# Kernel optimization log

Hardware: AMD Instinct MI355X
Metric: run time of the kernel (lower is better)

Reference implementation:

```python
import jax, jax.numpy as jnp
import numpy as np

EPSILON = 1e-6
SEARCH_RADIUS = 11 // 2  # search_window_size=11 -> 121 shifts
PATCH_RADIUS = 5 // 2    # patch_size=5 box sum


def shift_stack(t, r):
    # Matches ShiftStack: outer loop x_shift, inner loop y_shift, roll dims (H,W)=(2,3).
    # t: [B,C,H,W] -> [B,C,H,W,(2r+1)^2]
    return jnp.stack(
        [jnp.roll(t, (dy, dx), axis=(2, 3))
         for dx in range(-r, r + 1) for dy in range(-r, r + 1)],
        axis=-1,
    )


def box_sum(t, r):
    # Circular box-filter sum over a (2r+1)x(2r+1) window; separable form is
    # mathematically identical to the original 25 rolls (rolls commute/add).
    s = sum(jnp.roll(t, d, axis=2) for d in range(-r, r + 1))
    return sum(jnp.roll(s, d, axis=3) for d in range(-r, r + 1))


def setup_inputs() -> dict:
    key = jax.random.key(0)
    k1, k2 = jax.random.split(key)
    rgb = jax.random.uniform(k1, (1, 3, 512, 512), dtype=jnp.float32)
    # realistic noise std in [0.02, 0.12]
    sigma = jax.random.uniform(k2, (1, 1, 1, 1), dtype=jnp.float32) * 0.1 + 0.02
    return {"rgb": rgb, "sigma": sigma}


def reference(rgb, sigma):
    h = sigma * 2.0                                     # [B,1,1,1]
    y = 0.299 * rgb[:, :1] + 0.587 * rgb[:, 1:2] + 0.114 * rgb[:, 2:]  # [B,1,H,W]
    rgb_stack = shift_stack(rgb, SEARCH_RADIUS)         # [B,3,H,W,K]
    y_stack = shift_stack(y, SEARCH_RADIUS)             # [B,1,H,W,K]
    sq_diff = (y[..., None] - y_stack) ** 2             # [B,1,H,W,K]
    distances = jnp.sqrt(box_sum(sq_diff, PATCH_RADIUS))
    weights = jnp.exp(-distances / (jax.nn.relu(h)[..., None] + EPSILON))  # [B,1,H,W,K]
    denoised = (weights * rgb_stack).sum(axis=-1) / weights.sum(axis=-1)   # [B,3,H,W]
    return jnp.clip(denoised, 0.0, 1.0)
```

## Files before the change

### kernel.cpp

```cpp
#include <hip/hip_runtime.h>
#include <math.h>

#define IH 512
#define IW 512
#define NPX (IH*IW)

#define TW 60
#define BH 8
#define NXT 9
#define YROWS 22
#define YCOLS 74
#define YSZ2 (YROWS*YCOLS)

#define TS 32
#define YHALO 7
#define RHALO 5
#define YD (TS + 2*YHALO)
#define RD (TS + 2*RHALO)
#define RSZ (RD*RD)
#define MYSZ (YD*YD)

#define FSQRT(x) __builtin_amdgcn_sqrtf(x)
#if __has_builtin(__builtin_amdgcn_exp2f)
#define FEXP2(x) __builtin_amdgcn_exp2f(x)
#else
#define FEXP2(x) exp2f(x)
#endif

__device__ __forceinline__ float dpp_shl1(float x) {
    return __int_as_float(__builtin_amdgcn_update_dpp(
        0, __float_as_int(x), 0x130, 0xf, 0xf, true));
}

__global__ __launch_bounds__(256, 8)
void nlm_part(const float* __restrict__ rgb,
              const float* __restrict__ sigma,
              float4* __restrict__ ws) {
    __shared__ float YL[YSZ2];

    const int tid   = threadIdx.x;
    const int lane  = tid & 63;
    const int wavei = tid >> 6;
    const int tx0 = blockIdx.x * TW;
    const int ty0 = blockIdx.y * BH;
    const int slice = blockIdx.z;

    const float* Rp = rgb;
    const float* Gp = rgb + NPX;
    const float* Bp = rgb + 2*NPX;

    for (int idx = tid; idx < YSZ2; idx += 256) {
        int a = idx / YCOLS, b = idx - a*YCOLS;
        int gy = (ty0 + a - 7) & (IH-1);
        int gx = (tx0 + b - 7) & (IW-1);
        int g = gy*IW + gx;
        YL[idx] = 0.299f*Rp[g] + 0.587f*Gp[g] + 0.114f*Bp[g];
    }
    __syncthreads();

    const float m2 = -1.4426950408889634f /
                     (fmaxf(sigma[0]*2.0f, 0.0f) + 1e-6f);

    const int l  = lane;
    const int r0 = wavei*2;

    float yb6[6];
    #pragma unroll
    for (int i = 0; i < 6; ++i)
        yb6[i] = YL[(r0+5+i)*YCOLS + (l+5)];

    float accR[2]={0,0}, accG[2]={0,0}, accB[2]={0,0}, den[2]={0,0};

    const int dxlo  = (slice < 3) ? (-5 + 3*slice) : 4;
    const int dxcnt = (slice < 3) ? 3 : 2;

    for (int u = 0; u < dxcnt; ++u) {
        const int dx = dxlo + u;
        const int ysb  = r0*YCOLS + (l + 5 - dx);
        const int coli = (tx0 + l - dx) & (IW-1);

        float sub6[6];
        #pragma unroll
        for (int j = 0; j < 6; ++j)
            sub6[j] = YL[ysb + j*YCOLS];

        float rw[2], gw[2], bw[2];
        int oP = (((ty0 + r0 - 5) & (IH-1)) << 9) + coli;
        rw[0] = Rp[oP]; gw[0] = Gp[oP]; bw[0] = Bp[oP];
        oP = (oP + IW) & (NPX-1);

        #pragma unroll
        for (int k = 0; k <= 10; ++k) {
            rw[(k+1)&1] = Rp[oP];
            gw[(k+1)&1] = Gp[oP];
            bw[(k+1)&1] = Bp[oP];
            oP = (oP + IW) & (NPX-1);
            if (k > 0)
                sub6[(k+5)%6] = YL[ysb + (k+5)*YCOLS];

            float pre[7]; pre[0] = 0.f;
            #pragma unroll
            for (int i = 0; i < 6; ++i) {
                float d = yb6[i] - sub6[(i+k)%6];
                pre[i+1] = fmaf(d, d, pre[i]);
            }
            float V[2];
            V[0] = pre[5] - pre[0];
            V[1] = pre[6] - pre[1];

            float box[2];
            #pragma unroll
            for (int rr = 0; rr < 2; ++rr) {
                float s1 = dpp_shl1(V[rr]);
                float s2 = dpp_shl1(s1);
                float s3 = dpp_shl1(s2);
                float s4 = dpp_shl1(s3);
                box[rr] = ((V[rr] + s1) + (s2 + s3)) + s4;
            }
            #pragma unroll
            for (int rr = 0; rr < 2; ++rr) {
                float w = FEXP2(FSQRT(fmaxf(box[rr], 0.f)) * m2);
                accR[rr] = fmaf(w, rw[(k+rr)&1], accR[rr]);
                accG[rr] = fmaf(w, gw[(k+rr)&1], accG[rr]);
                accB[rr] = fmaf(w, bw[(k+rr)&1], accB[rr]);
                den[rr] += w;
            }
        }
    }

    if (l < TW && tx0 + l < IW) {
        #pragma unroll
        for (int rr = 0; rr < 2; ++rr) {
            int px = (ty0 + r0 + rr)*IW + tx0 + l;
            ws[(size_t)slice*NPX + px] =
                make_float4(accR[rr], accG[rr], accB[rr], den[rr]);
        }
    }
}

__global__ __launch_bounds__(256)
void nlm_combine(const float4* __restrict__ ws, float* __restrict__ out) {
    int px = blockIdx.x * 256 + threadIdx.x;
    float4 a = ws[px];
    float4 b = ws[NPX + px];
    float4 c = ws[2*(size_t)NPX + px];
    float4 d = ws[3*(size_t)NPX + px];
    float r  = (a.x + b.x) + (c.x + d.x);
    float g  = (a.y + b.y) + (c.y + d.y);
    float bl = (a.z + b.z) + (c.z + d.z);
    float w  = (a.w + b.w) + (c.w + d.w);
    float iw = 1.0f / w;
    out[px]           = fminf(fmaxf(r  * iw, 0.f), 1.f);
    out[NPX + px]     = fminf(fmaxf(g  * iw, 0.f), 1.f);
    out[2*NPX + px]   = fminf(fmaxf(bl * iw, 0.f), 1.f);
}

__global__ __launch_bounds__(256)
void nlm_mono(const float* __restrict__ rgb,
              const float* __restrict__ sigma,
              float* __restrict__ out) {
    __shared__ float Y[MYSZ];
    __shared__ float RGBL[3 * RSZ];

    const int tid = threadIdx.x;
    const int tx0 = blockIdx.x * TS;
    const int ty0 = blockIdx.y * TS;

    const float* Rp = rgb;
    const float* Gp = rgb + NPX;
    const float* Bp = rgb + 2 * NPX;

    for (int idx = tid; idx < MYSZ; idx += 256) {
        int a = idx / YD, b = idx - a * YD;
        int gy = (ty0 + a - YHALO) & (IH - 1);
        int gx = (tx0 + b - YHALO) & (IW - 1);
        int g = gy * IW + gx;
        Y[idx] = 0.299f * Rp[g] + 0.587f * Gp[g] + 0.114f * Bp[g];
    }
    for (int idx = tid; idx < RSZ; idx += 256) {
        int a = idx / RD, b = idx - a * RD;
        int gy = (ty0 + a - RHALO) & (IH - 1);
        int gx = (tx0 + b - RHALO) & (IW - 1);
        int g = gy * IW + gx;
        RGBL[idx]           = Rp[g];
        RGBL[RSZ + idx]     = Gp[g];
        RGBL[2 * RSZ + idx] = Bp[g];
    }
    __syncthreads();

    const float minv_h = -1.0f / (fmaxf(sigma[0] * 2.0f, 0.0f) + 1e-6f);
    const int tx = tid & 31;
    const int tz = tid >> 5;
    const int r0 = tz * 4;

    const int ybase = (YHALO + r0 - 2) * YD + (YHALO + tx - 2);
    float yb[8][5];
    #pragma unroll
    for (int i = 0; i < 8; ++i)
        #pragma unroll
        for (int b = 0; b < 5; ++b)
            yb[i][b] = Y[ybase + i * YD + b];

    float accR[4] = {0.f,0.f,0.f,0.f}, accG[4] = {0.f,0.f,0.f,0.f};
    float accB[4] = {0.f,0.f,0.f,0.f}, den[4] = {0.f,0.f,0.f,0.f};

    for (int dx = -5; dx <= 5; ++dx) {
        const int ybd = (YHALO + r0 - 7) * YD + (YHALO + tx - 2 - dx);
        const int rbd = (RHALO + r0 - 5) * RD + (RHALO + tx - dx);

        #pragma unroll
        for (int k = 0; k <= 10; ++k) {
            float hs[8];
            #pragma unroll
            for (int i = 0; i < 8; ++i) {
                float s = 0.f;
                #pragma unroll
                for (int b = 0; b < 5; ++b) {
                    float d = yb[i][b] - Y[ybd + (i + k) * YD + b];
                    s = fmaf(d, d, s);
                }
                hs[i] = s;
            }
            float pre[9];
            pre[0] = 0.f;
            #pragma unroll
            for (int i = 0; i < 8; ++i) pre[i + 1] = pre[i] + hs[i];
            #pragma unroll
            for (int rr = 0; rr < 4; ++rr) {
                float box = pre[rr + 5] - pre[rr];
                float w = __expf(FSQRT(box) * minv_h);
                const int s2 = rbd + (rr + k) * RD;
                accR[rr] = fmaf(w, RGBL[s2], accR[rr]);
                accG[rr] = fmaf(w, RGBL[RSZ + s2], accG[rr]);
                accB[rr] = fmaf(w, RGBL[2 * RSZ + s2], accB[rr]);
                den[rr] += w;
            }
        }
    }

    #pragma unroll
    for (int rr = 0; rr < 4; ++rr) {
        int px = (ty0 + r0 + rr) * IW + tx0 + tx;
        float iw = 1.0f / den[rr];
        out[px]           = fminf(fmaxf(accR[rr] * iw, 0.f), 1.f);
        out[NPX + px]     = fminf(fmaxf(accG[rr] * iw, 0.f), 1.f);
        out[2 * NPX + px] = fminf(fmaxf(accB[rr] * iw, 0.f), 1.f);
    }
}

extern "C" void kernel_launch(void* const* d_in, const int* in_sizes, int n_in,
                              void* d_out, int out_size, void* d_ws, size_t ws_size,
                              hipStream_t stream) {
    const float* rgb   = (const float*)d_in[0];
    const float* sigma = (const float*)d_in[1];
    float* out = (float*)d_out;

    const size_t need4 = (size_t)4 * NPX * sizeof(float4);
    if (ws_size >= need4) {
        float4* ws = (float4*)d_ws;
        dim3 grid(NXT, IH / BH, 4);
        nlm_part<<<grid, dim3(256), 0, stream>>>(rgb, sigma, ws);
        nlm_combine<<<dim3(NPX / 256), dim3(256), 0, stream>>>(ws, out);
    } else {
        dim3 grid(IW / TS, IH / TS);
        nlm_mono<<<grid, dim3(256), 0, stream>>>(rgb, sigma, out);
    }
}
```

Before: 36.28 us.

## Split dx shifts across six slices, interleaving two shifts per thread

The dx search range is now split into six grid slices instead of four. Five slices each process two adjacent dx shifts together inside the inner loop, and the last slice handles dx=5 alone. Interleaving two shifts gives the scheduler independent instruction streams for latency hiding, and the larger grid adds parallelism. In exchange, the combine kernel now reads six partial buffers, the workspace requirement grows, and the launch-bounds occupancy hint is dropped, which may raise register use.

```diff
diff --git a/kernel.cpp b/kernel.cpp
--- a/kernel.cpp
+++ b/kernel.cpp
@@ -32,7 +32,7 @@
         0, __float_as_int(x), 0x130, 0xf, 0xf, true));
 }
 
-__global__ __launch_bounds__(256, 8)
+__global__ __launch_bounds__(256)
 void nlm_part(const float* __restrict__ rgb,
               const float* __restrict__ sigma,
               float4* __restrict__ ws) {
@@ -71,11 +71,77 @@
 
     float accR[2]={0,0}, accG[2]={0,0}, accB[2]={0,0}, den[2]={0,0};
 
-    const int dxlo  = (slice < 3) ? (-5 + 3*slice) : 4;
-    const int dxcnt = (slice < 3) ? 3 : 2;
-
-    for (int u = 0; u < dxcnt; ++u) {
-        const int dx = dxlo + u;
+    if (slice < 5) {
+        const int dxa = -5 + 2*slice;
+        const int dxb = dxa + 1;
+        const int ysba  = r0*YCOLS + (l + 5 - dxa);
+        const int ysbb  = ysba - 1;
+        const int colia = (tx0 + l - dxa) & (IW-1);
+        const int colib = (tx0 + l - dxb) & (IW-1);
+
+        float subA[6], subB[6];
+        #pragma unroll
+        for (int j = 0; j < 6; ++j) {
+            subA[j] = YL[ysba + j*YCOLS];
+            subB[j] = YL[ysbb + j*YCOLS];
+        }
+
+        float rwA[2], gwA[2], bwA[2], rwB[2], gwB[2], bwB[2];
+        int rbse = ((ty0 + r0 - 5) & (IH-1)) << 9;
+        int oA = rbse + colia, oB = rbse + colib;
+        rwA[0] = Rp[oA]; gwA[0] = Gp[oA]; bwA[0] = Bp[oA];
+        rwB[0] = Rp[oB]; gwB[0] = Gp[oB]; bwB[0] = Bp[oB];
+        oA = (oA + IW) & (NPX-1);
+        oB = (oB + IW) & (NPX-1);
+
+        #pragma unroll
+        for (int k = 0; k <= 10; ++k) {
+            rwA[(k+1)&1] = Rp[oA]; gwA[(k+1)&1] = Gp[oA]; bwA[(k+1)&1] = Bp[oA];
+            rwB[(k+1)&1] = Rp[oB]; gwB[(k+1)&1] = Gp[oB]; bwB[(k+1)&1] = Bp[oB];
+            oA = (oA + IW) & (NPX-1);
+            oB = (oB + IW) & (NPX-1);
+            if (k > 0) {
+                subA[(k+5)%6] = YL[ysba + (k+5)*YCOLS];
+                subB[(k+5)%6] = YL[ysbb + (k+5)*YCOLS];
+            }
+            float pA[7], pB[7]; pA[0] = 0.f; pB[0] = 0.f;
+            #pragma unroll
+            for (int i = 0; i < 6; ++i) {
+                float da = yb6[i] - subA[(i+k)%6];
+                float db = yb6[i] - subB[(i+k)%6];
+                pA[i+1] = fmaf(da, da, pA[i]);
+                pB[i+1] = fmaf(db, db, pB[i]);
+            }
+            float VA[2], VB[2];
+            VA[0] = pA[5]-pA[0]; VA[1] = pA[6]-pA[1];
+            VB[0] = pB[5]-pB[0]; VB[1] = pB[6]-pB[1];
+
+            #pragma unroll
+            for (int rr = 0; rr < 2; ++rr) {
+                float a1 = dpp_shl1(VA[rr]);
+                float b1 = dpp_shl1(VB[rr]);
+                float a2 = dpp_shl1(a1);
+                float b2 = dpp_shl1(b1);
+                float a3 = dpp_shl1(a2);
+                float b3 = dpp_shl1(b2);
+                float a4 = dpp_shl1(a3);
+                float b4 = dpp_shl1(b3);
+                float boxA = ((VA[rr] + a1) + (a2 + a3)) + a4;
+                float boxB = ((VB[rr] + b1) + (b2 + b3)) + b4;
+                float wA = FEXP2(FSQRT(fmaxf(boxA, 0.f)) * m2);
+                float wB = FEXP2(FSQRT(fmaxf(boxB, 0.f)) * m2);
+                accR[rr] = fmaf(wA, rwA[(k+rr)&1], accR[rr]);
+                accG[rr] = fmaf(wA, gwA[(k+rr)&1], accG[rr]);
+                accB[rr] = fmaf(wA, bwA[(k+rr)&1], accB[rr]);
+                den[rr] += wA;
+                accR[rr] = fmaf(wB, rwB[(k+rr)&1], accR[rr]);
+                accG[rr] = fmaf(wB, gwB[(k+rr)&1], accG[rr]);
+                accB[rr] = fmaf(wB, bwB[(k+rr)&1], accB[rr]);
+                den[rr] += wB;
+            }
+        }
+    } else {
+        const int dx = 5;
         const int ysb  = r0*YCOLS + (l + 5 - dx);
         const int coli = (tx0 + l - dx) & (IW-1);
 
@@ -108,18 +174,14 @@
             V[0] = pre[5] - pre[0];
             V[1] = pre[6] - pre[1];
 
-            float box[2];
             #pragma unroll
             for (int rr = 0; rr < 2; ++rr) {
                 float s1 = dpp_shl1(V[rr]);
                 float s2 = dpp_shl1(s1);
                 float s3 = dpp_shl1(s2);
                 float s4 = dpp_shl1(s3);
-                box[rr] = ((V[rr] + s1) + (s2 + s3)) + s4;
-            }
-            #pragma unroll
-            for (int rr = 0; rr < 2; ++rr) {
-                float w = FEXP2(FSQRT(fmaxf(box[rr], 0.f)) * m2);
+                float box = ((V[rr] + s1) + (s2 + s3)) + s4;
+                float w = FEXP2(FSQRT(fmaxf(box, 0.f)) * m2);
                 accR[rr] = fmaf(w, rw[(k+rr)&1], accR[rr]);
                 accG[rr] = fmaf(w, gw[(k+rr)&1], accG[rr]);
                 accB[rr] = fmaf(w, bw[(k+rr)&1], accB[rr]);
@@ -141,18 +203,16 @@
 __global__ __launch_bounds__(256)
 void nlm_combine(const float4* __restrict__ ws, float* __restrict__ out) {
     int px = blockIdx.x * 256 + threadIdx.x;
-    float4 a = ws[px];
-    float4 b = ws[NPX + px];
-    float4 c = ws[2*(size_t)NPX + px];
-    float4 d = ws[3*(size_t)NPX + px];
-    float r  = (a.x + b.x) + (c.x + d.x);
-    float g  = (a.y + b.y) + (c.y + d.y);
-    float bl = (a.z + b.z) + (c.z + d.z);
-    float w  = (a.w + b.w) + (c.w + d.w);
+    float r = 0.f, g = 0.f, b = 0.f, w = 0.f;
+    #pragma unroll
+    for (int s = 0; s < 6; ++s) {
+        float4 v = ws[(size_t)s * NPX + px];
+        r += v.x; g += v.y; b += v.z; w += v.w;
+    }
     float iw = 1.0f / w;
-    out[px]           = fminf(fmaxf(r  * iw, 0.f), 1.f);
-    out[NPX + px]     = fminf(fmaxf(g  * iw, 0.f), 1.f);
-    out[2*NPX + px]   = fminf(fmaxf(bl * iw, 0.f), 1.f);
+    out[px]           = fminf(fmaxf(r * iw, 0.f), 1.f);
+    out[NPX + px]     = fminf(fmaxf(g * iw, 0.f), 1.f);
+    out[2*NPX + px]   = fminf(fmaxf(b * iw, 0.f), 1.f);
 }
 
 __global__ __launch_bounds__(256)
@@ -255,10 +315,10 @@
     const float* sigma = (const float*)d_in[1];
     float* out = (float*)d_out;
 
-    const size_t need4 = (size_t)4 * NPX * sizeof(float4);
-    if (ws_size >= need4) {
+    const size_t need6 = (size_t)6 * NPX * sizeof(float4);
+    if (ws_size >= need6) {
         float4* ws = (float4*)d_ws;
-        dim3 grid(NXT, IH / BH, 4);
+        dim3 grid(NXT, IH / BH, 6);
         nlm_part<<<grid, dim3(256), 0, stream>>>(rgb, sigma, ws);
         nlm_combine<<<dim3(NPX / 256), dim3(256), 0, stream>>>(ws, out);
     } else {
```

Measured after the change: 40.96 us. 12.9% more time.

## Pre-pack RGB into float4 and precompute luma in a separate kernel

Applied to the files above, without the earlier changes.

Adds a pre-pass kernel that interleaves the RGB planes into float4 pixels and writes a luma plane to workspace. The main kernel then fetches one 16-byte vector per neighbour row instead of three scalar loads, and its shared-memory tile load reads precomputed luma instead of recomputing it from three planes. The launch_bounds occupancy hint of 8 is dropped from nlm_part. This adds a third kernel launch, extra workspace and memory traffic, and a larger workspace requirement, so the tiled path is skipped if the workspace is too small.

```diff
diff --git a/kernel.cpp b/kernel.cpp
--- a/kernel.cpp
+++ b/kernel.cpp
@@ -32,8 +32,21 @@
         0, __float_as_int(x), 0x130, 0xf, 0xf, true));
 }
 
-__global__ __launch_bounds__(256, 8)
-void nlm_part(const float* __restrict__ rgb,
+__global__ __launch_bounds__(256)
+void nlm_pack(const float* __restrict__ rgb,
+              float4* __restrict__ pack,
+              float* __restrict__ Yg) {
+    int px = blockIdx.x * 256 + threadIdx.x;
+    float r = rgb[px];
+    float g = rgb[NPX + px];
+    float b = rgb[2*NPX + px];
+    pack[px] = make_float4(r, g, b, 0.f);
+    Yg[px]   = 0.299f*r + 0.587f*g + 0.114f*b;
+}
+
+__global__ __launch_bounds__(256)
+void nlm_part(const float4* __restrict__ pack,
+              const float* __restrict__ Yg,
               const float* __restrict__ sigma,
               float4* __restrict__ ws) {
     __shared__ float YL[YSZ2];
@@ -45,16 +58,11 @@
     const int ty0 = blockIdx.y * BH;
     const int slice = blockIdx.z;
 
-    const float* Rp = rgb;
-    const float* Gp = rgb + NPX;
-    const float* Bp = rgb + 2*NPX;
-
     for (int idx = tid; idx < YSZ2; idx += 256) {
         int a = idx / YCOLS, b = idx - a*YCOLS;
         int gy = (ty0 + a - 7) & (IH-1);
         int gx = (tx0 + b - 7) & (IW-1);
-        int g = gy*IW + gx;
-        YL[idx] = 0.299f*Rp[g] + 0.587f*Gp[g] + 0.114f*Bp[g];
+        YL[idx] = Yg[gy*IW + gx];
     }
     __syncthreads();
 
@@ -84,16 +92,14 @@
         for (int j = 0; j < 6; ++j)
             sub6[j] = YL[ysb + j*YCOLS];
 
-        float rw[2], gw[2], bw[2];
+        float4 rw[2];
         int oP = (((ty0 + r0 - 5) & (IH-1)) << 9) + coli;
-        rw[0] = Rp[oP]; gw[0] = Gp[oP]; bw[0] = Bp[oP];
+        rw[0] = pack[oP];
         oP = (oP + IW) & (NPX-1);
 
         #pragma unroll
         for (int k = 0; k <= 10; ++k) {
-            rw[(k+1)&1] = Rp[oP];
-            gw[(k+1)&1] = Gp[oP];
-            bw[(k+1)&1] = Bp[oP];
+            rw[(k+1)&1] = pack[oP];
             oP = (oP + IW) & (NPX-1);
             if (k > 0)
                 sub6[(k+5)%6] = YL[ysb + (k+5)*YCOLS];
@@ -120,9 +126,10 @@
             #pragma unroll
             for (int rr = 0; rr < 2; ++rr) {
                 float w = FEXP2(FSQRT(fmaxf(box[rr], 0.f)) * m2);
-                accR[rr] = fmaf(w, rw[(k+rr)&1], accR[rr]);
-                accG[rr] = fmaf(w, gw[(k+rr)&1], accG[rr]);
-                accB[rr] = fmaf(w, bw[(k+rr)&1], accB[rr]);
+                float4 p = rw[(k+rr)&1];
+                accR[rr] = fmaf(w, p.x, accR[rr]);
+                accG[rr] = fmaf(w, p.y, accG[rr]);
+                accB[rr] = fmaf(w, p.z, accB[rr]);
                 den[rr] += w;
             }
         }
@@ -255,11 +262,14 @@
     const float* sigma = (const float*)d_in[1];
     float* out = (float*)d_out;
 
-    const size_t need4 = (size_t)4 * NPX * sizeof(float4);
-    if (ws_size >= need4) {
-        float4* ws = (float4*)d_ws;
+    const size_t need = (size_t)5 * NPX * sizeof(float4) + (size_t)NPX * sizeof(float);
+    if (ws_size >= need) {
+        float4* ws   = (float4*)d_ws;
+        float4* pack = ws + (size_t)4 * NPX;
+        float*  Yg   = (float*)(ws + (size_t)5 * NPX);
+        nlm_pack<<<dim3(NPX / 256), dim3(256), 0, stream>>>(rgb, pack, Yg);
         dim3 grid(NXT, IH / BH, 4);
-        nlm_part<<<grid, dim3(256), 0, stream>>>(rgb, sigma, ws);
+        nlm_part<<<grid, dim3(256), 0, stream>>>(pack, Yg, sigma, ws);
         nlm_combine<<<dim3(NPX / 256), dim3(256), 0, stream>>>(ws, out);
     } else {
         dim3 grid(IW / TS, IH / TS);
```

After: 43.22 us. +19.1%, slower.
